# Kernel optimization log

Hardware: AMD Instinct MI355X
Metric: run time of the kernel (lower is better)

Reference implementation:

```python
import jax, jax.numpy as jnp
import numpy as np

L, B, D, N = 2048, 8, 1024, 64

def setup_inputs() -> dict:
    key = jax.random.key(0)
    ks = jax.random.split(key, 6)
    return {
        "x": jax.random.normal(ks[0], (L, B, D), dtype=jnp.float32),
        "damping_factor": jax.random.normal(ks[1], (D, N, 1), dtype=jnp.float32),
        "decay_factor": jax.random.normal(ks[2], (D, N, 1), dtype=jnp.float32),
        "ema_expansion_matrix": jax.random.normal(ks[3], (D, N, 1), dtype=jnp.float32),
        "kernel_projection_matrix": jax.random.normal(ks[4], (D, N), dtype=jnp.float32),
        "residual_weight": jax.random.normal(ks[5], (D,), dtype=jnp.float32),
    }

def reference(x, damping_factor, decay_factor, ema_expansion_matrix,
              kernel_projection_matrix, residual_weight):
    seq_len, bsz, dim = x.shape
    ndim = damping_factor.shape[1]
    # --- kernel synthesis (training path, unidirectional) ---
    damping = jax.nn.sigmoid(damping_factor)           # (D, N, 1)
    decay = jax.nn.sigmoid(decay_factor)               # (D, N, 1)
    prev_w = 1.0 - damping * decay                     # (D, N, 1), in (0,1)
    t = jnp.arange(seq_len, dtype=jnp.float32)[None, None, :]  # (1,1,L)
    vander = t * jnp.log(prev_w)                       # (D, N, L)
    kernel_vals = damping * ema_expansion_matrix * jnp.exp(vander)  # (D,N,L)
    kernel = jnp.einsum('dnl,dn->dl', kernel_vals, kernel_projection_matrix)
    kernel = kernel * np.float32(1.0 / np.sqrt(ndim))  # (D, L)
    # --- residual + FFT long convolution ---
    residual = x * residual_weight                     # (L, B, D)
    x_conv = jnp.transpose(x, (1, 2, 0))               # (B, D, L)
    n_fft = 2 * seq_len
    x_fft = jnp.fft.rfft(x_conv, n=n_fft)              # (B, D, n/2+1)
    k_fft = jnp.fft.rfft(kernel, n=n_fft)              # (D, n/2+1)
    conv = jnp.fft.irfft(x_fft * k_fft, n=n_fft)[..., :seq_len]  # (B, D, L)
    ema_out = jnp.transpose(conv, (2, 0, 1))           # (L, B, D)
    return jax.nn.silu(ema_out + residual)
```

## Files before the change

kernel.cpp:

```cpp
#include <hip/hip_runtime.h>
#include <hip/hip_bf16.h>


#define BSZ 8
#define DIM 1024
#define ND 64
#define BD 8192
#define SEGS 4
#define SEGLEN 512
#define CH1 64
#define CPS1 8
#define TD 16
#define XP1 68
#define NCH2 16
#define YP2 17

typedef short bf16x8 __attribute__((ext_vector_type(8)));
typedef float f32x4 __attribute__((ext_vector_type(4)));
union BF8 { uint32_t u[4]; bf16x8 v; };
#define MFMA __builtin_amdgcn_mfma_f32_16x16x32_bf16

__device__ __forceinline__ uint32_t pk_bf16(float a, float b) {
    __hip_bfloat162 h2 = __float22bfloat162_rn(make_float2(a, b));
    uint32_t u; __builtin_memcpy(&u, &h2, 4);
    return u;
}

__device__ __forceinline__ void block_sync_lds() {
    asm volatile("s_waitcnt lgkmcnt(0)" ::: "memory");
    __builtin_amdgcn_s_barrier();
    asm volatile("" ::: "memory");
}

__global__ __launch_bounds__(128, 8) void mega_pass1(
    const float* __restrict__ x,
    const float* __restrict__ dfp,
    const float* __restrict__ cfp,
    ushort* __restrict__ S)
{
    __shared__ float xb[2][TD * XP1];

    const int tid = threadIdx.x;
    const int lane = tid & 63;
    const int wv = tid >> 6;
    const int q   = (lane & 3) | (((lane >> 3) & 1) << 2);
    const int col = wv * 8 + ((lane >> 2) & 1) + ((lane >> 4) & 3) * 2;
    const int blk = blockIdx.x;
    const int dt  = blk & 63;
    const int b   = (blk >> 6) & 7;
    const int seg = blk >> 9;
    const int d   = dt * TD + col;

    float w[8];
    {
        const int pb = d * ND + q * 8;
        const float4 df0 = *(const float4*)(dfp + pb);
        const float4 df1 = *(const float4*)(dfp + pb + 4);
        const float4 cf0 = *(const float4*)(cfp + pb);
        const float4 cf1 = *(const float4*)(cfp + pb + 4);
        const float dfv[8] = {df0.x, df0.y, df0.z, df0.w, df1.x, df1.y, df1.z, df1.w};
        const float cfv[8] = {cf0.x, cf0.y, cf0.z, cf0.w, cf1.x, cf1.y, cf1.z, cf1.w};
        #pragma unroll
        for (int i = 0; i < 8; ++i) {
            const float sd = 1.0f / (1.0f + __expf(-dfv[i]));
            const float sc = 1.0f / (1.0f + __expf(-cfv[i]));
            w[i] = 1.0f - sd * sc;
        }
    }

    const int r0 = tid >> 2;
    const int c4 = (tid & 3) * 4;
    const float* xg = x + (size_t)(seg * SEGLEN) * BD + b * DIM + dt * TD;

    float4 nx0 = *(const float4*)(xg + (size_t)r0 * BD + c4);
    float4 nx1 = *(const float4*)(xg + (size_t)(r0 + 32) * BD + c4);

    float h[8];
    #pragma unroll
    for (int i = 0; i < 8; ++i) h[i] = 0.0f;

    for (int g = 0; g < CPS1; ++g) {
        float* xbuf = xb[g & 1];
        const float nv0[4] = {nx0.x, nx0.y, nx0.z, nx0.w};
        const float nv1[4] = {nx1.x, nx1.y, nx1.z, nx1.w};
        #pragma unroll
        for (int e = 0; e < 4; ++e) {
            xbuf[(c4 + e) * XP1 + r0]      = nv0[e];
            xbuf[(c4 + e) * XP1 + r0 + 32] = nv1[e];
        }
        if (g + 1 < CPS1) {
            nx0 = *(const float4*)(xg + (size_t)((g + 1) * CH1 + r0) * BD + c4);
            nx1 = *(const float4*)(xg + (size_t)((g + 1) * CH1 + r0 + 32) * BD + c4);
        }
        block_sync_lds();

        const float* xcol = xbuf + col * XP1;
        #pragma unroll 2
        for (int t8 = 0; t8 < 8; ++t8) {
            const float4 tva = *(const float4*)(xcol + t8 * 8);
            const float4 tvb = *(const float4*)(xcol + t8 * 8 + 4);
            const float tvs[8] = {tva.x, tva.y, tva.z, tva.w,
                                  tvb.x, tvb.y, tvb.z, tvb.w};
            #pragma unroll
            for (int k = 0; k < 8; ++k) {
                const float xv = tvs[k];
                #pragma unroll
                for (int i = 0; i < 8; ++i) h[i] = fmaf(w[i], h[i], xv);
            }
        }
    }

    const size_t sb = ((size_t)(seg * BSZ + b) * 64 + dt) * 1024 + col * 64 + q * 8;
    uint32_t pk[4] = {pk_bf16(h[0], h[1]), pk_bf16(h[2], h[3]),
                      pk_bf16(h[4], h[5]), pk_bf16(h[6], h[7])};
    *(uint4*)(S + sb) = make_uint4(pk[0], pk[1], pk[2], pk[3]);
}

__global__ __launch_bounds__(1024, 4) void mega_pass2(
    const float* __restrict__ x,
    const float* __restrict__ dfp,
    const float* __restrict__ cfp,
    const float* __restrict__ emp,
    const float* __restrict__ pjp,
    const float* __restrict__ rwp,
    const ushort* __restrict__ S,
    float* __restrict__ out)
{
    __shared__ __align__(16) float    xb[2][TD * 8 * 36];
    __shared__ __align__(16) float    yt[2][256 * YP2];
    __shared__ __align__(16) uint32_t hbq[16 * 256];
    __shared__ __align__(8)  float2   pclw[16 * 64];
    __shared__ float kap[16 * 32];

    const int tid = threadIdx.x;
    const int tl  = tid & 63;
    const int wv  = tid >> 6;
    const int c   = tl & 15;
    const int g   = tl >> 4;
    const int cq  = c & 7;
    const int hf  = c >> 3;
    const int blk = blockIdx.x;
    const int seg = blk >> 6;
    const int dt  = blk & 63;
    const int d0  = dt * TD;
    const int d   = d0 + wv;

    {
        const int pidx = d * ND + tl;
        const float sd = 1.0f / (1.0f + __expf(-dfp[pidx]));
        const float sc = 1.0f / (1.0f + __expf(-cfp[pidx]));
        const float wn = 1.0f - sd * sc;
        const float cn = sd * emp[pidx] * pjp[pidx] * 0.125f;
        pclw[wv * 64 + tl] = make_float2(cn, log2f(wn));
    }
    const float rwd = rwp[d];

    const int drow = tid & 15;
    const int bq   = (tid >> 4) & 7;
    const int l4g  = tid >> 7;
    const int gsw  = 4 * (l4g ^ (drow & 6));
    const int xwoff = (drow * 8 + bq) * 36 + gsw;
    const float* xgs = x + (size_t)(seg * SEGLEN + 4 * l4g) * BD + bq * DIM + d0 + drow;
    float nx0 = xgs[0];
    float nx1 = xgs[(size_t)BD];
    float nx2 = xgs[(size_t)2 * BD];
    float nx3 = xgs[(size_t)3 * BD];

    const int rid = tid >> 2;
    const int l_s = rid >> 3;
    const int b_s = rid & 7;
    const int dq  = tid & 3;
    const int yrho = b_s + 8 * ((l_s >> 2) & 3) + 32 * (l_s & 3) + 128 * (l_s >> 4);

    float lw16[16];
    #pragma unroll
    for (int T = 0; T < 4; ++T)
        #pragma unroll
        for (int r = 0; r < 4; ++r)
            lw16[T * 4 + r] = pclw[wv * 64 + 16 * T + 4 * g + r].y;

    float h[16];
    #pragma unroll
    for (int i = 0; i < 16; ++i) h[i] = 0.0f;
    if (seg > 0) {
        float w512[16];
        #pragma unroll
        for (int i = 0; i < 16; ++i) w512[i] = exp2f(512.0f * lw16[i]);
        for (int sp = 0; sp < seg; ++sp) {
            const size_t sbase = ((size_t)(sp * BSZ + cq) * 64 + dt) * 1024 + wv * 64;
            #pragma unroll
            for (int T = 0; T < 4; ++T) {
                const uint2 u = *(const uint2*)(S + sbase + 16 * T + 4 * g);
                const float s0 = __uint_as_float(u.x << 16);
                const float s1 = __uint_as_float(u.x & 0xFFFF0000u);
                const float s2 = __uint_as_float(u.y << 16);
                const float s3 = __uint_as_float(u.y & 0xFFFF0000u);
                h[T*4+0] = fmaf(w512[T*4+0], h[T*4+0], s0);
                h[T*4+1] = fmaf(w512[T*4+1], h[T*4+1], s1);
                h[T*4+2] = fmaf(w512[T*4+2], h[T*4+2], s2);
                h[T*4+3] = fmaf(w512[T*4+3], h[T*4+3], s3);
            }
        }
    }
    float w32[16];
    #pragma unroll
    for (int i = 0; i < 16; ++i) w32[i] = exp2f(32.0f * lw16[i]);

    BF8 Vf[4], T2f[2][2], Kf[2];
    #pragma unroll
    for (int T = 0; T < 4; ++T) {
        const float2 pcl = pclw[wv * 64 + 16 * T + c];
        const float winv = exp2f(-pcl.y);
        float ve = exp2f((float)(31 - 8 * g) * pcl.y);
        float vv[8];
        #pragma unroll
        for (int e = 0; e < 8; ++e) { vv[e] = ve; ve *= winv; }
        #pragma unroll
        for (int j = 0; j < 4; ++j) Vf[T].u[j] = pk_bf16(vv[2*j], vv[2*j+1]);
    }
    #pragma unroll
    for (int Tk = 0; Tk < 2; ++Tk) {
        float2 m8[8];
        #pragma unroll
        for (int e = 0; e < 8; ++e) m8[e] = pclw[wv * 64 + 32 * Tk + 8 * g + e];
        #pragma unroll
        for (int Tj = 0; Tj < 2; ++Tj) {
            const float jf = (float)(16 * Tj + c + 1);
            float tv[8];
            #pragma unroll
            for (int e = 0; e < 8; ++e) tv[e] = m8[e].x * exp2f(jf * m8[e].y);
            #pragma unroll
            for (int j = 0; j < 4; ++j) T2f[Tj][Tk].u[j] = pk_bf16(tv[2*j], tv[2*j+1]);
        }
    }
    {
        const int p = tl >> 1, half = tl & 1;
        float acc = 0.0f;
        for (int i = 0; i < 32; ++i) {
            const float2 pc = pclw[wv * 64 + half * 32 + i];
            acc = fmaf(pc.x, exp2f((float)p * pc.y), acc);
        }
        const int prt = __builtin_amdgcn_update_dpp(0, __float_as_int(acc), 0xB1, 0xF, 0xF, true);
        acc += __int_as_float(prt);
        if (!half) kap[wv * 32 + p] = acc;
    }
    #pragma unroll
    for (int Tj = 0; Tj < 2; ++Tj) {
        float kv[8];
        #pragma unroll
        for (int e = 0; e < 8; ++e) {
            const int pp = 16 * Tj + c - 8 * g - e;
            const float kr = kap[wv * 32 + (pp > 0 ? pp : 0)];
            kv[e] = (pp >= 0) ? kr : 0.0f;
        }
        #pragma unroll
        for (int j = 0; j < 4; ++j) Kf[Tj].u[j] = pk_bf16(kv[2*j], kv[2*j+1]);
    }

    const int sgm = wv & 6;
    const int kb  = 4 * ((2 * g) ^ sgm);
    const int jb  = 4 * ((4 * hf + g) ^ sgm);
    const int swzc = ((c & 3) << 3) | (((c >> 2) & 1) << 2);
    uint32_t* hbw = hbq + wv * 256 + cq * 32;
    float* ogbase = out + (size_t)(seg * SEGLEN) * BD + d0;
    const f32x4 zf = {0.0f, 0.0f, 0.0f, 0.0f};

    if (hf == 0) {
        #pragma unroll
        for (int T = 0; T < 4; ++T) {
            const int p0 = 8 * T + 2 * g;
            *(uint2*)(&hbw[p0 ^ swzc]) =
                make_uint2(pk_bf16(h[4*T+0], h[4*T+1]), pk_bf16(h[4*T+2], h[4*T+3]));
        }
    }
    {
        *(float4*)(&xb[0][xwoff]) = make_float4(nx0, nx1, nx2, nx3);
        const float* xp = xgs + (size_t)32 * BD;
        nx0 = xp[0]; nx1 = xp[(size_t)BD]; nx2 = xp[(size_t)2*BD]; nx3 = xp[(size_t)3*BD];
    }
    block_sync_lds();

    for (int ch = 0; ch < NCH2; ++ch) {
        const float* xrow = xb[ch & 1] + (wv * 8 + cq) * 36;

        BF8 hB0, hB1;
        {
            const uint4 a  = *(const uint4*)(&hbw[(4 * g) ^ swzc]);
            const uint4 b2 = *(const uint4*)(&hbw[(16 + 4 * g) ^ swzc]);
            hB0.u[0]=a.x;  hB0.u[1]=a.y;  hB0.u[2]=a.z;  hB0.u[3]=a.w;
            hB1.u[0]=b2.x; hB1.u[1]=b2.y; hB1.u[2]=b2.z; hB1.u[3]=b2.w;
        }
        BF8 xB;
        {
            const float4 fa = *(const float4*)(xrow + kb);
            const float4 fb = *(const float4*)(xrow + kb + 4);
            xB.u[0] = pk_bf16(fa.x, fa.y); xB.u[1] = pk_bf16(fa.z, fa.w);
            xB.u[2] = pk_bf16(fb.x, fb.y); xB.u[3] = pk_bf16(fb.z, fb.w);
        }

        if (ch + 1 < NCH2) {
            *(float4*)(&xb[(ch + 1) & 1][xwoff]) = make_float4(nx0, nx1, nx2, nx3);
            if (ch + 2 < NCH2) {
                const float* xp = xgs + (size_t)(ch + 2) * 32 * BD;
                nx0 = xp[0]; nx1 = xp[(size_t)BD]; nx2 = xp[(size_t)2*BD]; nx3 = xp[(size_t)3*BD];
            }
        }
        if (ch > 0) {
            const float* yprev = yt[(ch - 1) & 1];
            float ov[4];
            #pragma unroll
            for (int e = 0; e < 4; ++e) ov[e] = yprev[yrho * YP2 + 4 * dq + e];
            *(float4*)(ogbase + (size_t)((ch - 1) * 32 + l_s) * BD + b_s * DIM + 4 * dq) =
                make_float4(ov[0], ov[1], ov[2], ov[3]);
        }

        f32x4 y0 = MFMA(Kf[0].v, xB.v, zf, 0, 0, 0);
        f32x4 y1 = MFMA(Kf[1].v, xB.v, zf, 0, 0, 0);
        y0 = MFMA(T2f[0][0].v, hB0.v, y0, 0, 0, 0);
        y1 = MFMA(T2f[1][0].v, hB0.v, y1, 0, 0, 0);
        y0 = MFMA(T2f[0][1].v, hB1.v, y0, 0, 0, 0);
        y1 = MFMA(T2f[1][1].v, hB1.v, y1, 0, 0, 0);
        #pragma unroll
        for (int T = 0; T < 4; ++T) {
            const f32x4 U = MFMA(Vf[T].v, xB.v, zf, 0, 0, 0);
            h[4*T+0] = fmaf(w32[4*T+0], h[4*T+0], U[0]);
            h[4*T+1] = fmaf(w32[4*T+1], h[4*T+1], U[1]);
            h[4*T+2] = fmaf(w32[4*T+2], h[4*T+2], U[2]);
            h[4*T+3] = fmaf(w32[4*T+3], h[4*T+3], U[3]);
        }
        if (hf == 0) {
            #pragma unroll
            for (int T = 0; T < 4; ++T) {
                const int p0 = 8 * T + 2 * g;
                *(uint2*)(&hbw[p0 ^ swzc]) =
                    make_uint2(pk_bf16(h[4*T+0], h[4*T+1]), pk_bf16(h[4*T+2], h[4*T+3]));
            }
        }

        {
            float* ycur = yt[ch & 1];
            const float4 xres = *(const float4*)(xrow + jb);
            const float xr[4] = {xres.x, xres.y, xres.z, xres.w};
            const f32x4 yy = hf ? y1 : y0;
            #pragma unroll
            for (int r = 0; r < 4; ++r) {
                const float v = yy[r] + rwd * xr[r];
                const float sv = v / (1.0f + __expf(-v));
                ycur[(cq + 8 * (g + 4 * r + 16 * hf)) * YP2 + wv] = sv;
            }
        }
        block_sync_lds();
    }

    {
        const float* yprev = yt[(NCH2 - 1) & 1];
        float ov[4];
        #pragma unroll
        for (int e = 0; e < 4; ++e) ov[e] = yprev[yrho * YP2 + 4 * dq + e];
        *(float4*)(ogbase + (size_t)((NCH2 - 1) * 32 + l_s) * BD + b_s * DIM + 4 * dq) =
            make_float4(ov[0], ov[1], ov[2], ov[3]);
    }
}

extern "C" void kernel_launch(void* const* d_in, const int* in_sizes, int n_in,
                              void* d_out, int out_size, void* d_ws, size_t ws_size,
                              hipStream_t stream) {
    const float* x  = (const float*)d_in[0];
    const float* df = (const float*)d_in[1];
    const float* cf = (const float*)d_in[2];
    const float* em = (const float*)d_in[3];
    const float* pj = (const float*)d_in[4];
    const float* rw = (const float*)d_in[5];
    float* out = (float*)d_out;
    ushort* S  = (ushort*)d_ws;

    mega_pass1<<<dim3((SEGS - 1) * BSZ * 64), dim3(128), 0, stream>>>(x, df, cf, S);
    mega_pass2<<<dim3(SEGS * 64), dim3(1024), 0, stream>>>(x, df, cf, em, pj, rw, S, out);
}
```

Baseline: 75.19 us.

## Halve pass2 channel tile to 8 and double grid with swizzled block mapping

Pass 2 now processes 8 channels per block with 512 threads instead of 16 with 1024, doubling the grid from 256 to 512 blocks. Shared-memory buffers and the thread-to-data index maps shrink to match. Block indices are swizzled so adjacent channel tiles come from the same pass-1 tile, with an adjusted S offset. The aim is better occupancy and CU coverage on a GPU with 256 CUs, at the cost of less reuse per block and more redundant per-block setup.

```diff
diff --git a/kernel.cpp b/kernel.cpp
--- a/kernel.cpp
+++ b/kernel.cpp
@@ -10,10 +10,11 @@
 #define SEGLEN 512
 #define CH1 64
 #define CPS1 8
-#define TD 16
+#define TD1 16
 #define XP1 68
 #define NCH2 16
-#define YP2 17
+#define TD2 8
+#define YP2 9
 
 typedef short bf16x8 __attribute__((ext_vector_type(8)));
 typedef float f32x4 __attribute__((ext_vector_type(4)));
@@ -38,7 +39,7 @@
     const float* __restrict__ cfp,
     ushort* __restrict__ S)
 {
-    __shared__ float xb[2][TD * XP1];
+    __shared__ float xb[2][TD1 * XP1];
 
     const int tid = threadIdx.x;
     const int lane = tid & 63;
@@ -49,7 +50,7 @@
     const int dt  = blk & 63;
     const int b   = (blk >> 6) & 7;
     const int seg = blk >> 9;
-    const int d   = dt * TD + col;
+    const int d   = dt * TD1 + col;
 
     float w[8];
     {
@@ -70,7 +71,7 @@
 
     const int r0 = tid >> 2;
     const int c4 = (tid & 3) * 4;
-    const float* xg = x + (size_t)(seg * SEGLEN) * BD + b * DIM + dt * TD;
+    const float* xg = x + (size_t)(seg * SEGLEN) * BD + b * DIM + dt * TD1;
 
     float4 nx0 = *(const float4*)(xg + (size_t)r0 * BD + c4);
     float4 nx1 = *(const float4*)(xg + (size_t)(r0 + 32) * BD + c4);
@@ -116,7 +117,7 @@
     *(uint4*)(S + sb) = make_uint4(pk[0], pk[1], pk[2], pk[3]);
 }
 
-__global__ __launch_bounds__(1024, 4) void mega_pass2(
+__global__ __launch_bounds__(512, 4) void mega_pass2(
     const float* __restrict__ x,
     const float* __restrict__ dfp,
     const float* __restrict__ cfp,
@@ -126,11 +127,11 @@
     const ushort* __restrict__ S,
     float* __restrict__ out)
 {
-    __shared__ __align__(16) float    xb[2][TD * 8 * 36];
+    __shared__ __align__(16) float    xb[2][TD2 * 8 * 36];
     __shared__ __align__(16) float    yt[2][256 * YP2];
-    __shared__ __align__(16) uint32_t hbq[16 * 256];
-    __shared__ __align__(8)  float2   pclw[16 * 64];
-    __shared__ float kap[16 * 32];
+    __shared__ __align__(16) uint32_t hbq[TD2 * 256];
+    __shared__ __align__(8)  float2   pclw[TD2 * 64];
+    __shared__ float kap[TD2 * 32];
 
     const int tid = threadIdx.x;
     const int tl  = tid & 63;
@@ -140,9 +141,12 @@
     const int cq  = c & 7;
     const int hf  = c >> 3;
     const int blk = blockIdx.x;
-    const int seg = blk >> 6;
-    const int dt  = blk & 63;
-    const int d0  = dt * TD;
+    const int x8  = blk & 7;
+    const int qq  = blk >> 3;
+    const int pairid = x8 * 32 + (qq >> 1);
+    const int seg = pairid >> 6;
+    const int dt  = ((pairid & 63) << 1) | (qq & 1);
+    const int d0  = dt * TD2;
     const int d   = d0 + wv;
 
     {
@@ -155,9 +159,9 @@
     }
     const float rwd = rwp[d];
 
-    const int drow = tid & 15;
-    const int bq   = (tid >> 4) & 7;
-    const int l4g  = tid >> 7;
+    const int drow = tid & 7;
+    const int bq   = (tid >> 3) & 7;
+    const int l4g  = tid >> 6;
     const int gsw  = 4 * (l4g ^ (drow & 6));
     const int xwoff = (drow * 8 + bq) * 36 + gsw;
     const float* xgs = x + (size_t)(seg * SEGLEN + 4 * l4g) * BD + bq * DIM + d0 + drow;
@@ -166,11 +170,11 @@
     float nx2 = xgs[(size_t)2 * BD];
     float nx3 = xgs[(size_t)3 * BD];
 
-    const int rid = tid >> 2;
+    const int rid = tid >> 1;
     const int l_s = rid >> 3;
     const int b_s = rid & 7;
-    const int dq  = tid & 3;
-    const int yrho = b_s + 8 * ((l_s >> 2) & 3) + 32 * (l_s & 3) + 128 * (l_s >> 4);
+    const int dq  = tid & 1;
+    const int yrho = b_s + 8 * (((l_s >> 2) & 3) + 4 * (l_s & 3) + 16 * (l_s >> 4));
 
     float lw16[16];
     #pragma unroll
@@ -186,8 +190,9 @@
         float w512[16];
         #pragma unroll
         for (int i = 0; i < 16; ++i) w512[i] = exp2f(512.0f * lw16[i]);
+        const int scol = ((dt & 1) << 3) + wv;
         for (int sp = 0; sp < seg; ++sp) {
-            const size_t sbase = ((size_t)(sp * BSZ + cq) * 64 + dt) * 1024 + wv * 64;
+            const size_t sbase = ((size_t)(sp * BSZ + cq) * 64 + (dt >> 1)) * 1024 + scol * 64;
             #pragma unroll
             for (int T = 0; T < 4; ++T) {
                 const uint2 u = *(const uint2*)(S + sbase + 16 * T + 4 * g);
@@ -375,5 +380,5 @@
     ushort* S  = (ushort*)d_ws;
 
     mega_pass1<<<dim3((SEGS - 1) * BSZ * 64), dim3(128), 0, stream>>>(x, df, cf, S);
-    mega_pass2<<<dim3(SEGS * 64), dim3(1024), 0, stream>>>(x, df, cf, em, pj, rw, S, out);
-}
+    mega_pass2<<<dim3(SEGS * (DIM / TD2)), dim3(512), 0, stream>>>(x, df, cf, em, pj, rw, S, out);
+}
```

Measured after the change: 76.49 us. About the same (+1.7%).
